# Optimization experiments

Measured on AMD Instinct MI355X. Metric: run time of the kernel, lower is better.

The kernel has to match this reference:

```python
import jax, jax.numpy as jnp
import numpy as np

B, T, D, R = 128, 1024, 8, 512
ALPHA = 0.7
BETA_PLUS = 0.5 * (1.0 - ALPHA)   # 0.15, superdiagonal (circulant)
BETA_MINUS = 0.5 * (1.0 + ALPHA)  # 0.85, subdiagonal (circulant)


def setup_inputs() -> dict:
    key = jax.random.key(0)
    k1, k2 = jax.random.split(key)
    x = jax.random.normal(k1, (B, T, D), dtype=jnp.float32)
    # torch init: uniform_(a=0.0, b=1.0) on input_projection.weight [R, D]
    W_in = jax.random.uniform(k2, (R, D), dtype=jnp.float32)
    return {"x": x, "W_in": W_in}


def reference(x, W_in):
    # u = input_projection(x): [B, T, R]
    u = jnp.einsum("btd,rd->btr", x, W_in)

    def step(state, u_t):
        # state_projection with circulant beta matrix; state @ A^T equals:
        # 0.15*roll(state,-1) + 0.85*roll(state,+1) along reservoir dim
        pre = (BETA_PLUS * jnp.roll(state, -1, axis=-1)
               + BETA_MINUS * jnp.roll(state, 1, axis=-1)
               + u_t)
        new_state = jnp.tanh(pre)  # leaking_rate = 0.0 -> pure new state
        return new_state, new_state

    s0 = jnp.zeros((u.shape[0], u.shape[2]), dtype=u.dtype)
    # torch loop: t in range(1, T) -> consumes u[:, 1:, :]; u[:, 0] unused
    _, states = jax.lax.scan(step, s0, jnp.swapaxes(u[:, 1:, :], 0, 1))
    states = jnp.swapaxes(states, 0, 1)  # [B, T-1, R]
    # returned slice all_states[:, 1:, :] has an all-zero final timestep
    tail = jnp.zeros((u.shape[0], 1, u.shape[2]), dtype=u.dtype)
    return jnp.concatenate([states, tail], axis=1)  # [B, T, R]
```

## Files before the change

### kernel.cpp

```cpp
#include <hip/hip_runtime.h>


#define B_DIM 128
#define T_DIM 1024
#define D_DIM 8
#define R_DIM 512
#define NT    16
#define NPHASE 64

#define SC   2.8853900817779268f
#define BP_S (0.15f * SC)
#define BM_S (0.85f * SC)

__device__ __forceinline__ float esn_step(float L, float R, float u) {
    const float pre = fmaf(BM_S, L, fmaf(BP_S, R, u));
#if __has_builtin(__builtin_amdgcn_exp2f) && __has_builtin(__builtin_amdgcn_rcpf)
    const float e = __builtin_amdgcn_exp2f(pre);
    return fmaf(-2.0f, __builtin_amdgcn_rcpf(e + 1.0f), 1.0f);
#else
    const float e = exp2f(pre);
    return 1.0f - 2.0f / (e + 1.0f);
#endif
}

__device__ __forceinline__ float dpp_prev(float v) {
    return __uint_as_float((unsigned)__builtin_amdgcn_update_dpp(
        0, (int)__float_as_uint(v), 0x111, 0xf, 0xf, true));
}
__device__ __forceinline__ float dpp_next(float v) {
    return __uint_as_float((unsigned)__builtin_amdgcn_update_dpp(
        0, (int)__float_as_uint(v), 0x101, 0xf, 0xf, true));
}

__device__ __forceinline__ void barrier_lds_only() {
    asm volatile("s_waitcnt lgkmcnt(0)\n\ts_barrier" ::: "memory");
}

__global__ __launch_bounds__(512, 1) void esn_kernel(const float* __restrict__ x,
                                                     const float* __restrict__ W,
                                                     float* __restrict__ out) {
    __shared__ float ubuf[2][NT][R_DIM];
    __shared__ float S[2][R_DIM];

    const int b   = blockIdx.x;
    const int tid = threadIdx.x;
    const float* xb = x + (size_t)b * T_DIM * D_DIM;

    const float4 wa = *(const float4*)(W + tid * D_DIM);
    const float4 wc = *(const float4*)(W + tid * D_DIM + 4);
    const float w0 = wa.x * SC, w1 = wa.y * SC, w2 = wa.z * SC, w3 = wa.w * SC;
    const float w4 = wc.x * SC, w5 = wc.y * SC, w6 = wc.z * SC, w7 = wc.w * SC;

#pragma unroll
    for (int j = 0; j < NT; ++j) {
        const float4 xa = *(const float4*)(xb + (j + 1) * D_DIM);
        const float4 xc = *(const float4*)(xb + (j + 1) * D_DIM + 4);
        float u = xa.x * w0;
        u = fmaf(xa.y, w1, u); u = fmaf(xa.z, w2, u); u = fmaf(xa.w, w3, u);
        u = fmaf(xc.x, w4, u); u = fmaf(xc.y, w5, u);
        u = fmaf(xc.z, w6, u); u = fmaf(xc.w, w7, u);
        ubuf[0][j][tid] = u;
    }
    __syncthreads();

    const int wid  = tid >> 6;
    const int lane = tid & 63;

    if (wid < 4) {
        asm volatile("s_setprio 3" ::: "memory");
        const int q  = lane >> 4;
        const int p  = lane & 15;
        const int r0 = (128 * wid + 32 * q - 16 + 4 * p) & (R_DIM - 1);
        const bool core = (p >= 4) && (p < 12);

        float s0 = 0.0f, s1 = 0.0f, s2 = 0.0f, s3 = 0.0f;
        float* op = out + (size_t)b * T_DIM * R_DIM + r0;

        for (int k = 0; k < NPHASE; ++k) {
            const float* ub = &ubuf[k & 1][0][r0];
            const int steps = (k == NPHASE - 1) ? (1023 - NT * (NPHASE - 1)) : NT;
            float4 ua = *(const float4*)ub;
            for (int tl = 0; tl < steps; ++tl) {
                const int tn = (tl + 1 < steps) ? (tl + 1) : tl;
                const float4 na = *(const float4*)(ub + (size_t)tn * R_DIM);

                const float Lh = dpp_prev(s3);
                const float Rh = dpp_next(s0);

                const float n1 = esn_step(s0, s2, ua.y);
                const float n2 = esn_step(s1, s3, ua.z);
                const float n0 = esn_step(Lh, s1, ua.x);
                const float n3 = esn_step(s2, Rh, ua.w);

                if (core) *(float4*)op = make_float4(n0, n1, n2, n3);
                op += R_DIM;

                s0 = n0; s1 = n1; s2 = n2; s3 = n3;
                ua = na;
            }
            if (core) *(float4*)&S[k & 1][r0] = make_float4(s0, s1, s2, s3);
            barrier_lds_only();
            const float4 sv = *(const float4*)&S[k & 1][r0];
            s0 = sv.x; s1 = sv.y; s2 = sv.z; s3 = sv.w;
        }
    } else {
        asm volatile("s_setprio 0" ::: "memory");
        const int pid = tid - 256;
        const int pr  = 2 * pid;
        const float4 Aa = *(const float4*)(W + pr * D_DIM);
        const float4 Ac = *(const float4*)(W + pr * D_DIM + 4);
        const float4 Ba = *(const float4*)(W + (pr + 1) * D_DIM);
        const float4 Bc = *(const float4*)(W + (pr + 1) * D_DIM + 4);
        const float a0 = Aa.x * SC, a1 = Aa.y * SC, a2 = Aa.z * SC, a3 = Aa.w * SC;
        const float a4 = Ac.x * SC, a5 = Ac.y * SC, a6 = Ac.z * SC, a7 = Ac.w * SC;
        const float c0 = Ba.x * SC, c1 = Ba.y * SC, c2 = Ba.z * SC, c3 = Ba.w * SC;
        const float c4 = Bc.x * SC, c5 = Bc.y * SC, c6 = Bc.z * SC, c7 = Bc.w * SC;

        for (int k = 0; k < NPHASE; ++k) {
            if (k + 1 < NPHASE) {
                const int tb = NT * (k + 1) + 1;
                float* dst = &ubuf[(k + 1) & 1][0][0];
#pragma unroll
                for (int tl = 0; tl < NT; ++tl) {
                    const int t = tb + tl;
                    if (t < T_DIM) {
                        const float4 xa = *(const float4*)(xb + t * D_DIM);
                        const float4 xc = *(const float4*)(xb + t * D_DIM + 4);
                        float u0 = xa.x * a0;
                        u0 = fmaf(xa.y, a1, u0); u0 = fmaf(xa.z, a2, u0);
                        u0 = fmaf(xa.w, a3, u0); u0 = fmaf(xc.x, a4, u0);
                        u0 = fmaf(xc.y, a5, u0); u0 = fmaf(xc.z, a6, u0);
                        u0 = fmaf(xc.w, a7, u0);
                        float u1 = xa.x * c0;
                        u1 = fmaf(xa.y, c1, u1); u1 = fmaf(xa.z, c2, u1);
                        u1 = fmaf(xa.w, c3, u1); u1 = fmaf(xc.x, c4, u1);
                        u1 = fmaf(xc.y, c5, u1); u1 = fmaf(xc.z, c6, u1);
                        u1 = fmaf(xc.w, c7, u1);
                        *(float2*)&dst[tl * R_DIM + pr] = make_float2(u0, u1);
                    }
                }
            }
            barrier_lds_only();
        }
    }

    out[(size_t)b * T_DIM * R_DIM + (size_t)(T_DIM - 1) * R_DIM + tid] = 0.0f;
}

extern "C" void kernel_launch(void* const* d_in, const int* in_sizes, int n_in,
                              void* d_out, int out_size, void* d_ws, size_t ws_size,
                              hipStream_t stream) {
    const float* x = (const float*)d_in[0];
    const float* W = (const float*)d_in[1];
    float* out = (float*)d_out;

    esn_kernel<<<dim3(B_DIM), dim3(512), 0, stream>>>(x, W, out);
}
```

Before: 347.6 us.

## Fuse input projection into recurrence and use all 8 waves with 2 elems/lane

Drops the producer/consumer split in which four waves computed the input projection into an LDS double buffer. Now all 512 threads run the recurrence, each owning 2 reservoir elements with halo overlap. Each thread computes its own projection inline from x loaded straight from global, with a 2-step register prefetch. The halo exchange through LDS and the barrier now happen every 8 steps instead of every 16. This removes the LDS staging of u and halves the per-lane serial work per step, at the cost of more frequent barriers, redundant projection FMAs on the critical path, and per-step global loads of x.

Measured after the change: 536.0 us. +54.2%, slower.

```diff
diff --git a/kernel.cpp b/kernel.cpp
--- a/kernel.cpp
+++ b/kernel.cpp
@@ -5,8 +5,7 @@
 #define T_DIM 1024
 #define D_DIM 8
 #define R_DIM 512
-#define NT    16
-#define NPHASE 64
+#define NTH   8
 
 #define SC   2.8853900817779268f
 #define BP_S (0.15f * SC)
@@ -39,108 +38,68 @@
 __global__ __launch_bounds__(512, 1) void esn_kernel(const float* __restrict__ x,
                                                      const float* __restrict__ W,
                                                      float* __restrict__ out) {
-    __shared__ float ubuf[2][NT][R_DIM];
     __shared__ float S[2][R_DIM];
 
     const int b   = blockIdx.x;
     const int tid = threadIdx.x;
     const float* xb = x + (size_t)b * T_DIM * D_DIM;
 
-    const float4 wa = *(const float4*)(W + tid * D_DIM);
-    const float4 wc = *(const float4*)(W + tid * D_DIM + 4);
-    const float w0 = wa.x * SC, w1 = wa.y * SC, w2 = wa.z * SC, w3 = wa.w * SC;
-    const float w4 = wc.x * SC, w5 = wc.y * SC, w6 = wc.z * SC, w7 = wc.w * SC;
+    const int j  = tid >> 4;
+    const int p  = tid & 15;
+    const int r0 = (16 * j - 8 + 2 * p) & (R_DIM - 1);
+    const bool core = (p >= 4) && (p < 12);
 
-#pragma unroll
-    for (int j = 0; j < NT; ++j) {
-        const float4 xa = *(const float4*)(xb + (j + 1) * D_DIM);
-        const float4 xc = *(const float4*)(xb + (j + 1) * D_DIM + 4);
-        float u = xa.x * w0;
-        u = fmaf(xa.y, w1, u); u = fmaf(xa.z, w2, u); u = fmaf(xa.w, w3, u);
-        u = fmaf(xc.x, w4, u); u = fmaf(xc.y, w5, u);
-        u = fmaf(xc.z, w6, u); u = fmaf(xc.w, w7, u);
-        ubuf[0][j][tid] = u;
-    }
-    __syncthreads();
+    const float4 A0 = *(const float4*)(W + r0 * D_DIM);
+    const float4 A1 = *(const float4*)(W + r0 * D_DIM + 4);
+    const float4 B0 = *(const float4*)(W + (r0 + 1) * D_DIM);
+    const float4 B1 = *(const float4*)(W + (r0 + 1) * D_DIM + 4);
+    const float a0 = A0.x * SC, a1 = A0.y * SC, a2 = A0.z * SC, a3 = A0.w * SC;
+    const float a4 = A1.x * SC, a5 = A1.y * SC, a6 = A1.z * SC, a7 = A1.w * SC;
+    const float c0 = B0.x * SC, c1 = B0.y * SC, c2 = B0.z * SC, c3 = B0.w * SC;
+    const float c4 = B1.x * SC, c5 = B1.y * SC, c6 = B1.z * SC, c7 = B1.w * SC;
 
-    const int wid  = tid >> 6;
-    const int lane = tid & 63;
+    float s0 = 0.0f, s1 = 0.0f;
+    float* op = out + (size_t)b * T_DIM * R_DIM + r0;
 
-    if (wid < 4) {
-        asm volatile("s_setprio 3" ::: "memory");
-        const int q  = lane >> 4;
-        const int p  = lane & 15;
-        const int r0 = (128 * wid + 32 * q - 16 + 4 * p) & (R_DIM - 1);
-        const bool core = (p >= 4) && (p < 12);
+    float4 xa0 = *(const float4*)(xb + D_DIM);
+    float4 xc0 = *(const float4*)(xb + D_DIM + 4);
+    float4 xa1 = *(const float4*)(xb + 2 * D_DIM);
+    float4 xc1 = *(const float4*)(xb + 2 * D_DIM + 4);
 
-        float s0 = 0.0f, s1 = 0.0f, s2 = 0.0f, s3 = 0.0f;
-        float* op = out + (size_t)b * T_DIM * R_DIM + r0;
+    int par = 0;
+    for (int i = 0; i < T_DIM - 1; ++i) {
+        int tp = i + 3; if (tp > T_DIM - 1) tp = T_DIM - 1;
+        const float4 pa = *(const float4*)(xb + tp * D_DIM);
+        const float4 pc = *(const float4*)(xb + tp * D_DIM + 4);
 
-        for (int k = 0; k < NPHASE; ++k) {
-            const float* ub = &ubuf[k & 1][0][r0];
-            const int steps = (k == NPHASE - 1) ? (1023 - NT * (NPHASE - 1)) : NT;
-            float4 ua = *(const float4*)ub;
-            for (int tl = 0; tl < steps; ++tl) {
-                const int tn = (tl + 1 < steps) ? (tl + 1) : tl;
-                const float4 na = *(const float4*)(ub + (size_t)tn * R_DIM);
+        float u0 = xa0.x * a0;
+        u0 = fmaf(xa0.y, a1, u0); u0 = fmaf(xa0.z, a2, u0);
+        u0 = fmaf(xa0.w, a3, u0); u0 = fmaf(xc0.x, a4, u0);
+        u0 = fmaf(xc0.y, a5, u0); u0 = fmaf(xc0.z, a6, u0);
+        u0 = fmaf(xc0.w, a7, u0);
+        float u1 = xa0.x * c0;
+        u1 = fmaf(xa0.y, c1, u1); u1 = fmaf(xa0.z, c2, u1);
+        u1 = fmaf(xa0.w, c3, u1); u1 = fmaf(xc0.x, c4, u1);
+        u1 = fmaf(xc0.y, c5, u1); u1 = fmaf(xc0.z, c6, u1);
+        u1 = fmaf(xc0.w, c7, u1);
 
-                const float Lh = dpp_prev(s3);
-                const float Rh = dpp_next(s0);
+        const float Lh = dpp_prev(s1);
+        const float Rh = dpp_next(s0);
 
-                const float n1 = esn_step(s0, s2, ua.y);
-                const float n2 = esn_step(s1, s3, ua.z);
-                const float n0 = esn_step(Lh, s1, ua.x);
-                const float n3 = esn_step(s2, Rh, ua.w);
+        const float n0 = esn_step(Lh, s1, u0);
+        const float n1 = esn_step(s0, Rh, u1);
 
-                if (core) *(float4*)op = make_float4(n0, n1, n2, n3);
-                op += R_DIM;
+        if (core) *(float2*)op = make_float2(n0, n1);
+        op += R_DIM;
+        s0 = n0; s1 = n1;
+        xa0 = xa1; xc0 = xc1; xa1 = pa; xc1 = pc;
 
-                s0 = n0; s1 = n1; s2 = n2; s3 = n3;
-                ua = na;
-            }
-            if (core) *(float4*)&S[k & 1][r0] = make_float4(s0, s1, s2, s3);
+        if ((i & (NTH - 1)) == (NTH - 1)) {
+            if (core) *(float2*)&S[par][r0] = make_float2(s0, s1);
             barrier_lds_only();
-            const float4 sv = *(const float4*)&S[k & 1][r0];
-            s0 = sv.x; s1 = sv.y; s2 = sv.z; s3 = sv.w;
-        }
-    } else {
-        asm volatile("s_setprio 0" ::: "memory");
-        const int pid = tid - 256;
-        const int pr  = 2 * pid;
-        const float4 Aa = *(const float4*)(W + pr * D_DIM);
-        const float4 Ac = *(const float4*)(W + pr * D_DIM + 4);
-        const float4 Ba = *(const float4*)(W + (pr + 1) * D_DIM);
-        const float4 Bc = *(const float4*)(W + (pr + 1) * D_DIM + 4);
-        const float a0 = Aa.x * SC, a1 = Aa.y * SC, a2 = Aa.z * SC, a3 = Aa.w * SC;
-        const float a4 = Ac.x * SC, a5 = Ac.y * SC, a6 = Ac.z * SC, a7 = Ac.w * SC;
-        const float c0 = Ba.x * SC, c1 = Ba.y * SC, c2 = Ba.z * SC, c3 = Ba.w * SC;
-        const float c4 = Bc.x * SC, c5 = Bc.y * SC, c6 = Bc.z * SC, c7 = Bc.w * SC;
-
-        for (int k = 0; k < NPHASE; ++k) {
-            if (k + 1 < NPHASE) {
-                const int tb = NT * (k + 1) + 1;
-                float* dst = &ubuf[(k + 1) & 1][0][0];
-#pragma unroll
-                for (int tl = 0; tl < NT; ++tl) {
-                    const int t = tb + tl;
-                    if (t < T_DIM) {
-                        const float4 xa = *(const float4*)(xb + t * D_DIM);
-                        const float4 xc = *(const float4*)(xb + t * D_DIM + 4);
-                        float u0 = xa.x * a0;
-                        u0 = fmaf(xa.y, a1, u0); u0 = fmaf(xa.z, a2, u0);
-                        u0 = fmaf(xa.w, a3, u0); u0 = fmaf(xc.x, a4, u0);
-                        u0 = fmaf(xc.y, a5, u0); u0 = fmaf(xc.z, a6, u0);
-                        u0 = fmaf(xc.w, a7, u0);
-                        float u1 = xa.x * c0;
-                        u1 = fmaf(xa.y, c1, u1); u1 = fmaf(xa.z, c2, u1);
-                        u1 = fmaf(xa.w, c3, u1); u1 = fmaf(xc.x, c4, u1);
-                        u1 = fmaf(xc.y, c5, u1); u1 = fmaf(xc.z, c6, u1);
-                        u1 = fmaf(xc.w, c7, u1);
-                        *(float2*)&dst[tl * R_DIM + pr] = make_float2(u0, u1);
-                    }
-                }
-            }
-            barrier_lds_only();
+            const float2 sv = *(const float2*)&S[par][r0];
+            s0 = sv.x; s1 = sv.y;
+            par ^= 1;
         }
     }
 
```
